# Kernel tuning notes

Hardware: AMD Instinct MI355X
Metric: run time of the kernel (lower is better)

Reference implementation:

```python
import jax, jax.numpy as jnp
import numpy as np

QTZ_BETA = 0.25


def setup_inputs() -> dict:
    key = jax.random.key(0)
    k1, k2 = jax.random.split(key)
    z = jax.random.normal(k1, (65536, 1, 256), dtype=jnp.float32)
    codebook = jax.random.normal(k2, (4096, 256), dtype=jnp.float32)
    return {"z": z, "codebook": codebook}


def reference(z, codebook):
    """Hard VQ quantization: nearest-codebook lookup with straight-through
    estimator plus codebook commitment loss. Returns (z_q, codebook_loss,
    min_embed_ids)."""
    D = codebook.shape[-1]
    z_f = z.reshape(-1, D)  # [N, D]
    # Pairwise squared L2 distances via expansion: ||z||^2 - 2 z c^T + ||c||^2
    # (argmin is invariant to the monotone transform vs. torch.cdist's sqrt)
    d2 = (
        jnp.sum(z_f * z_f, axis=1, keepdims=True)  # [N, 1]
        - 2.0 * (z_f @ codebook.T)                 # [N, K]
        + jnp.sum(codebook * codebook, axis=1)     # [K]
    )
    min_embed_ids = jnp.argmin(d2, axis=1)  # [N]
    # one_hot @ codebook is exactly a gather of codebook rows
    z_q = jnp.take(codebook, min_embed_ids, axis=0).reshape(z.shape)
    # Straight-through estimator
    z_q = z + jax.lax.stop_gradient(z_q - z)
    # Codebook loss (uses the STE z_q, matching the torch code)
    codebook_loss = (
        jnp.mean((jax.lax.stop_gradient(z_q) - z) ** 2)
        + jnp.mean((z_q - jax.lax.stop_gradient(z)) ** 2) * QTZ_BETA
    )
    return (z_q, codebook_loss, min_embed_ids)
```

## Files before the change

### kernel.cpp

```cpp
#include <hip/hip_runtime.h>
#include <stdint.h>

typedef _Float16 f16;
typedef _Float16 f16x4 __attribute__((ext_vector_type(4)));
typedef _Float16 f16x8 __attribute__((ext_vector_type(8)));
typedef float f32x4 __attribute__((ext_vector_type(4)));
typedef unsigned long long u64;

#define D_DIM 256
#define K_CB 4096
#define N_ROWS 65536
#define BM 128
#define BN 128
#define N_TILES 32
#define LOSS_OFF 16777216
#define IDS_OFF 16777217
#define MAX_FIX 4096

#define WS_CHI 0
#define WS_CN 2097152
#define WS_CNT 2113536
#define WS_ROWS 2113600
#define WS_SLOTS 2129984

#define LDS_BYTES 81920

#define GL_LDS(g, s_) __builtin_amdgcn_global_load_lds( \
    (const __attribute__((address_space(1))) void*)(g), \
    (__attribute__((address_space(3))) void*)(s_), 16, 0, 0)

static __device__ __forceinline__ uint32_t f2u(float x) { union { float f; uint32_t u; } c; c.f = x; return c.u; }
static __device__ __forceinline__ float u2f(uint32_t x) { union { float f; uint32_t u; } c; c.u = x; return c.f; }
static __device__ __forceinline__ uint32_t umin_(uint32_t a, uint32_t b) { return a < b ? a : b; }
static __device__ __forceinline__ uint32_t umax_(uint32_t a, uint32_t b) { return a > b ? a : b; }
static __device__ __forceinline__ u64 d2u(double x) { union { double d; u64 u; } c; c.d = x; return c.u; }

static __device__ __forceinline__ uint32_t med3u(uint32_t a, uint32_t b, uint32_t c) {
    uint32_t d;
    asm("v_med3_u32 %0, %1, %2, %3" : "=v"(d) : "v"(a), "v"(b), "v"(c));
    return d;
}
static __device__ __forceinline__ uint32_t min3u(uint32_t a, uint32_t b, uint32_t c) {
    uint32_t d;
    asm("v_min3_u32 %0, %1, %2, %3" : "=v"(d) : "v"(a), "v"(b), "v"(c));
    return d;
}

#define INS3(s_, kk_) do { \
    const uint32_t kkv_ = (kk_); \
    const uint32_t n1_ = umin_(k1[s_], kkv_); \
    const uint32_t n2_ = med3u(kkv_, k1[s_], k2[s_]); \
    const uint32_t n3_ = med3u(kkv_, k2[s_], k3[s_]); \
    k1[s_] = n1_; k2[s_] = n2_; k3[s_] = n3_; \
} while (0)

__global__ __launch_bounds__(256) void k_prep_cb(const float* __restrict__ cb,
                                                 f16* __restrict__ chi,
                                                 float* __restrict__ cn,
                                                 uint32_t* __restrict__ cnt,
                                                 u64* __restrict__ slots,
                                                 float* __restrict__ loss_slot) {
    const int tid = threadIdx.x;
    const int w = tid >> 6, l = tid & 63;
    const int row = blockIdx.x * 4 + w;
    const float4 v = ((const float4*)cb)[row * 64 + l];
    f16x4 h4;
    h4[0] = (f16)v.x; h4[1] = (f16)v.y; h4[2] = (f16)v.z; h4[3] = (f16)v.w;
    float ss = v.x * v.x + v.y * v.y + v.z * v.z + v.w * v.w;
#pragma unroll
    for (int m = 32; m >= 1; m >>= 1) ss += __shfl_xor(ss, m);
    ((f16x4*)chi)[row * 64 + l] = h4;
    if (l == 0) cn[row] = ss;
    if (tid < 4) slots[blockIdx.x * 4 + tid] = 0xFFFFFFFFFFFFFFFFull;
    if (blockIdx.x == 0 && tid == 0) { *cnt = 0; *loss_slot = 0.0f; }
}

__global__ __launch_bounds__(512, 4) void k_main(const float* __restrict__ z,
                                                 const float* __restrict__ cb,
                                                 const f16* __restrict__ chi,
                                                 const float* __restrict__ cn,
                                                 uint32_t* __restrict__ cnt,
                                                 uint32_t* __restrict__ rows,
                                                 float* __restrict__ out) {
    extern __shared__ char smem[];
    const int tid = threadIdx.x;
    const int w = tid >> 6, l = tid & 63;
    const int wm = w >> 1, wn = w & 1;
    const int l15 = l & 15, qh = l >> 4;
    const int blk = blockIdx.x;
    const float* ztile = z + (size_t)blk * (BM * D_DIM);

    const int e0 = tid >> 2;
    const int q0 = (tid & 3) ^ ((e0 >> 1) & 3);
    const int offE = e0 * 256 + q0 * 8;

    {
        const f16* gh = chi + offE;
        char* bb = smem + 65536 + w * 1024;
        GL_LDS(gh, bb);
    }

#pragma unroll 4
    for (int p = 0; p < 16; ++p) {
        const int r = p * 8 + w;
        const float4 v = ((const float4*)ztile)[r * 64 + l];
        f16x4 h4;
        h4[0] = (f16)(v.x * -2.0f); h4[1] = (f16)(v.y * -2.0f);
        h4[2] = (f16)(v.z * -2.0f); h4[3] = (f16)(v.w * -2.0f);
        const int kcw = l >> 3, q = (l >> 1) & 3, half = l & 1;
        const int addr = kcw * 8192 + r * 64 + (((q ^ ((r >> 1) & 3))) << 4) + half * 8;
        *(f16x4*)(smem + addr) = h4;
    }

    float cnNext[4];
#pragma unroll
    for (int j = 0; j < 4; ++j) cnNext[j] = cn[wn * 64 + j * 16 + l15];

    const int ab = wm * 2048 + l15 * 64 + ((qh ^ ((l15 >> 1) & 3)) << 4);

    int bcon[4];
#pragma unroll
    for (int j = 0; j < 4; ++j) {
        const int e = wn * 64 + j * 16 + l15;
        bcon[j] = e * 64 + ((qh ^ ((e >> 1) & 3)) << 4);
    }

    uint32_t k1[8], k2[8], k3[8];
#pragma unroll
    for (int s = 0; s < 8; ++s) { k1[s] = 0xFFFFFFFFu; k2[s] = 0xFFFFFFFFu; k3[s] = 0xFFFFFFFFu; }

    f32x4 acc[2][4];

    __syncthreads();

    for (int tile = 0; tile < N_TILES; ++tile) {
#pragma unroll
        for (int j = 0; j < 4; ++j) {
            const float base = cnNext[j] + 64.0f;
#pragma unroll
            for (int i = 0; i < 2; ++i) acc[i][j] = (f32x4){base, base, base, base};
        }
#pragma unroll
        for (int kc = 0; kc < 8; ++kc) {
            const int step = tile * 8 + kc;
            asm volatile("s_waitcnt vmcnt(0)" ::: "memory");
            __builtin_amdgcn_s_barrier();
            __builtin_amdgcn_sched_barrier(0);
            if (step + 1 < N_TILES * 8) {
                const int nt = (step + 1) >> 3, nk = (step + 1) & 7;
                const f16* gh = chi + nt * (BN * D_DIM) + nk * 32 + offE;
                char* bb = smem + 65536 + ((kc + 1) & 1) * 8192 + w * 1024;
                GL_LDS(gh, bb);
            }
            if (kc == 0) {
                const int tn = (tile + 1 < N_TILES) ? tile + 1 : tile;
#pragma unroll
                for (int j = 0; j < 4; ++j)
                    cnNext[j] = cn[tn * BN + wn * 64 + j * 16 + l15];
            }
            const char* bbase = smem + 65536 + (kc & 1) * 8192;
            f16x8 ah[2], bh[4];
#pragma unroll
            for (int i = 0; i < 2; ++i)
                ah[i] = *(const f16x8*)(smem + ab + kc * 8192 + i * 1024);
#pragma unroll
            for (int j = 0; j < 4; ++j) bh[j] = *(const f16x8*)(bbase + bcon[j]);
#pragma unroll
            for (int i = 0; i < 2; ++i)
#pragma unroll
                for (int j = 0; j < 4; ++j)
                    acc[i][j] = __builtin_amdgcn_mfma_f32_16x16x32_f16(ah[i], bh[j], acc[i][j], 0, 0, 0);
        }
        const int colb = tile * BN + wn * 64 + l15;
#pragma unroll
        for (int j = 0; j < 4; ++j) {
            const uint32_t col = (uint32_t)(colb + j * 16);
#pragma unroll
            for (int i = 0; i < 2; ++i)
#pragma unroll
                for (int rr = 0; rr < 4; ++rr) {
                    const uint32_t kk = (f2u(acc[i][j][rr]) & 0xFFFFF000u) | col;
                    INS3(i * 4 + rr, kk);
                }
        }
    }

#pragma unroll
    for (int s = 0; s < 8; ++s) {
        uint32_t a1 = k1[s], a2 = k2[s], a3 = k3[s];
#pragma unroll
        for (int m = 1; m <= 8; m <<= 1) {
            const uint32_t b1 = (uint32_t)__shfl_xor((int)a1, m);
            const uint32_t b2 = (uint32_t)__shfl_xor((int)a2, m);
            const uint32_t b3 = (uint32_t)__shfl_xor((int)a3, m);
            const uint32_t r1 = umin_(a1, b1);
            const uint32_t r2 = min3u(a2, b2, umax_(a1, b1));
            const uint32_t r3 = min3u(umax_(a1, b2), umax_(a2, b1), umin_(a3, b3));
            a1 = r1; a2 = r2; a3 = r3;
        }
        k1[s] = a1; k2[s] = a2; k3[s] = a3;
    }
    __syncthreads();
    uint32_t* mk = (uint32_t*)(smem + 65536);
    double* lossW = (double*)(smem + 65536 + 1536);
    if (wn == 0 && l15 == 0) {
#pragma unroll
        for (int s = 0; s < 8; ++s) {
            const int row = wm * 32 + (s >> 2) * 16 + qh * 4 + (s & 3);
            mk[row] = k1[s]; mk[128 + row] = k2[s]; mk[256 + row] = k3[s];
        }
    }
    __syncthreads();
    if (wn == 1 && l15 == 0) {
#pragma unroll
        for (int s = 0; s < 8; ++s) {
            const int row = wm * 32 + (s >> 2) * 16 + qh * 4 + (s & 3);
            const uint32_t b1 = mk[row], b2 = mk[128 + row], b3 = mk[256 + row];
            mk[row] = umin_(k1[s], b1);
            mk[128 + row] = min3u(k2[s], b2, umax_(k1[s], b1));
            mk[256 + row] = min3u(umax_(k1[s], b2), umax_(k2[s], b1), umin_(k3[s], b3));
        }
    }
    __syncthreads();

    double lossAcc = 0.0;
    for (int it = 0; it < 16; ++it) {
        const int row = it * 8 + w;
        const uint32_t K1 = mk[row], K2 = mk[128 + row], K3 = mk[256 + row];
        const int col1 = (int)(K1 & 4095u), col2 = (int)(K2 & 4095u);
        const float4 c1 = ((const float4*)cb)[col1 * 64 + l];
        const float4 c2 = ((const float4*)cb)[col2 * 64 + l];
        const float4 z4 = ((const float4*)ztile)[row * 64 + l];
        double e1, e2;
        {
            const double dx1 = (double)c1.x - z4.x, dy1 = (double)c1.y - z4.y;
            const double dz1 = (double)c1.z - z4.z, dw1 = (double)c1.w - z4.w;
            e1 = dx1 * dx1 + dy1 * dy1 + dz1 * dz1 + dw1 * dw1;
            const double dx2 = (double)c2.x - z4.x, dy2 = (double)c2.y - z4.y;
            const double dz2 = (double)c2.z - z4.z, dw2 = (double)c2.w - z4.w;
            e2 = dx2 * dx2 + dy2 * dy2 + dz2 * dz2 + dw2 * dw2;
        }
        float zn2 = z4.x * z4.x + z4.y * z4.y + z4.z * z4.z + z4.w * z4.w;
#pragma unroll
        for (int m = 32; m >= 1; m >>= 1) {
            e1 += __shfl_xor(e1, m);
            e2 += __shfl_xor(e2, m);
            zn2 += __shfl_xor(zn2, m);
        }
        const bool take1 = (e1 < e2) || (e1 == e2 && col1 <= col2);
        const float4 cw = take1 ? c1 : c2;
        ((float4*)out)[(blk * BM + row) * 64 + l] = cw;
        if (l == 0) {
            const int colw = take1 ? col1 : col2;
            const double ew = take1 ? e1 : e2;
            out[IDS_OFF + blk * BM + row] = (float)colw;
            lossAcc += ew;
            const float d3 = u2f(K3 & 0xFFFFF000u) + zn2 - 64.0f;
            const float eps = 0.006f * sqrtf(zn2) + 0.01f;
            if (!((float)ew < d3 - eps)) {
                const uint32_t e = atomicAdd(cnt, 1u);
                if (e < MAX_FIX) rows[e] = (uint32_t)(blk * BM + row);
            }
        }
    }
    if (l == 0) lossW[w] = lossAcc;
    __syncthreads();
    if (tid == 0) {
        double tot = 0.0;
#pragma unroll
        for (int i = 0; i < 8; ++i) tot += lossW[i];
        atomicAdd(out + LOSS_OFF, (float)(tot * (1.25 / 16777216.0)));
    }
}

__global__ __launch_bounds__(256) void k_fix_scan(const float* __restrict__ z,
                                                  const float* __restrict__ cb,
                                                  const uint32_t* __restrict__ cnt,
                                                  const uint32_t* __restrict__ rows,
                                                  u64* __restrict__ slots) {
    __shared__ float zrow[256];
    __shared__ u64 wmin[4];
    const int tid = threadIdx.x;
    const int w = tid >> 6, l = tid & 63;
    const int chunk = blockIdx.x & 15;
    uint32_t n = *cnt; if (n > MAX_FIX) n = MAX_FIX;
    for (uint32_t e = blockIdx.x >> 4; e < n; e += 64) {
        const int row = (int)rows[e];
        __syncthreads();
        if (tid < 64) ((float4*)zrow)[tid] = ((const float4*)z)[row * 64 + tid];
        __syncthreads();
        const int c = chunk * 256 + tid;
        const float4* crow = (const float4*)(cb + (size_t)c * 256);
        double s = 0.0;
        for (int q = 0; q < 64; ++q) {
            const float4 cv = crow[q];
            const float4 zv = ((const float4*)zrow)[q];
            const double dx = (double)cv.x - zv.x, dy = (double)cv.y - zv.y;
            const double dz = (double)cv.z - zv.z, dw = (double)cv.w - zv.w;
            s += dx * dx + dy * dy + dz * dz + dw * dw;
        }
        u64 key = (d2u(s) & 0xFFFFFFFFFFFFF000ull) | (u64)c;
#pragma unroll
        for (int m = 32; m >= 1; m >>= 1) {
            const u64 o = __shfl_xor(key, m);
            if (o < key) key = o;
        }
        if (l == 0) wmin[w] = key;
        __syncthreads();
        if (tid == 0) {
            u64 k = wmin[0];
            if (wmin[1] < k) k = wmin[1];
            if (wmin[2] < k) k = wmin[2];
            if (wmin[3] < k) k = wmin[3];
            atomicMin(&slots[e], k);
        }
    }
}

__global__ __launch_bounds__(256) void k_fix_patch(const float* __restrict__ z,
                                                   const float* __restrict__ cb,
                                                   const uint32_t* __restrict__ cnt,
                                                   const uint32_t* __restrict__ rows,
                                                   const u64* __restrict__ slots,
                                                   float* __restrict__ out) {
    const int tid = threadIdx.x;
    uint32_t n = *cnt; if (n > MAX_FIX) n = MAX_FIX;
    for (uint32_t e = blockIdx.x; e < n; e += 256) {
        const int row = (int)rows[e];
        const int newc = (int)(slots[e] & 4095ull);
        const int oldc = (int)out[IDS_OFF + row];
        if (newc == oldc) continue;
        double dOld = 0.0, dNew = 0.0;
        if (tid < 64) {
            const float4 zv = ((const float4*)z)[row * 64 + tid];
            const float4 co = ((const float4*)cb)[oldc * 64 + tid];
            const float4 cn4 = ((const float4*)cb)[newc * 64 + tid];
            const double ax = (double)co.x - zv.x, ay = (double)co.y - zv.y;
            const double az = (double)co.z - zv.z, aw = (double)co.w - zv.w;
            dOld = ax * ax + ay * ay + az * az + aw * aw;
            const double bx = (double)cn4.x - zv.x, by = (double)cn4.y - zv.y;
            const double bz = (double)cn4.z - zv.z, bw = (double)cn4.w - zv.w;
            dNew = bx * bx + by * by + bz * bz + bw * bw;
            ((float4*)out)[row * 64 + tid] = cn4;
        }
#pragma unroll
        for (int m = 32; m >= 1; m >>= 1) {
            dOld += __shfl_xor(dOld, m);
            dNew += __shfl_xor(dNew, m);
        }
        if (tid == 0) {
            out[IDS_OFF + row] = (float)newc;
            atomicAdd(out + LOSS_OFF, (float)((dNew - dOld) * (1.25 / 16777216.0)));
        }
    }
}

extern "C" void kernel_launch(void* const* d_in, const int* in_sizes, int n_in,
                              void* d_out, int out_size, void* d_ws, size_t ws_size,
                              hipStream_t stream) {
    (void)in_sizes; (void)n_in; (void)out_size; (void)ws_size;
    const float* z = (const float*)d_in[0];
    const float* cb = (const float*)d_in[1];
    float* out = (float*)d_out;
    char* ws = (char*)d_ws;
    f16* chi = (f16*)(ws + WS_CHI);
    float* cn = (float*)(ws + WS_CN);
    uint32_t* cnt = (uint32_t*)(ws + WS_CNT);
    uint32_t* rows = (uint32_t*)(ws + WS_ROWS);
    u64* slots = (u64*)(ws + WS_SLOTS);

    hipFuncSetAttribute((const void*)k_main,
                        hipFuncAttributeMaxDynamicSharedMemorySize, LDS_BYTES);

    k_prep_cb<<<K_CB / 4, 256, 0, stream>>>(cb, chi, cn, cnt, slots, out + LOSS_OFF);
    k_main<<<N_ROWS / BM, 512, LDS_BYTES, stream>>>(z, cb, chi, cn, cnt, rows, out);
    k_fix_scan<<<1024, 256, 0, stream>>>(z, cb, cnt, rows, slots);
    k_fix_patch<<<256, 256, 0, stream>>>(z, cb, cnt, rows, slots, out);
}
```

Baseline: 290.2 us.

## Use 16 waves per block with 4-stage codebook prefetch and LDS norms

Doubles the block to 1024 threads (16 waves in a 4x4 layout), so each wave computes a 32x32 sub-tile instead of 32x64. The codebook half-precision stream moves from double buffering to a 4-slot ring with prefetch three steps ahead and a relaxed vmcnt wait. All 4096 codebook norms are staged once in LDS rather than reloaded from global memory each tile. The top-3 candidate merge is extended across four column-waves with extra barriers. LDS use grows to 112 KB, which limits residency to one block per CU and halves the per-wave MFMA work between barriers.

```diff
diff --git a/kernel.cpp b/kernel.cpp
--- a/kernel.cpp
+++ b/kernel.cpp
@@ -23,7 +23,10 @@
 #define WS_ROWS 2113600
 #define WS_SLOTS 2129984
 
-#define LDS_BYTES 81920
+#define B_BASE 0
+#define CN_BASE 32768
+#define A_BASE 49152
+#define LDS_BYTES 114688
 
 #define GL_LDS(g, s_) __builtin_amdgcn_global_load_lds( \
     (const __attribute__((address_space(1))) void*)(g), \
@@ -75,17 +78,17 @@
     if (blockIdx.x == 0 && tid == 0) { *cnt = 0; *loss_slot = 0.0f; }
 }
 
-__global__ __launch_bounds__(512, 4) void k_main(const float* __restrict__ z,
-                                                 const float* __restrict__ cb,
-                                                 const f16* __restrict__ chi,
-                                                 const float* __restrict__ cn,
-                                                 uint32_t* __restrict__ cnt,
-                                                 uint32_t* __restrict__ rows,
-                                                 float* __restrict__ out) {
+__global__ __launch_bounds__(1024, 4) void k_main(const float* __restrict__ z,
+                                                  const float* __restrict__ cb,
+                                                  const f16* __restrict__ chi,
+                                                  const float* __restrict__ cn,
+                                                  uint32_t* __restrict__ cnt,
+                                                  uint32_t* __restrict__ rows,
+                                                  float* __restrict__ out) {
     extern __shared__ char smem[];
     const int tid = threadIdx.x;
     const int w = tid >> 6, l = tid & 63;
-    const int wm = w >> 1, wn = w & 1;
+    const int wm = w >> 2, wn = w & 3;
     const int l15 = l & 15, qh = l >> 4;
     const int blk = blockIdx.x;
     const float* ztile = z + (size_t)blk * (BM * D_DIM);
@@ -94,86 +97,81 @@
     const int q0 = (tid & 3) ^ ((e0 >> 1) & 3);
     const int offE = e0 * 256 + q0 * 8;
 
-    {
-        const f16* gh = chi + offE;
-        char* bb = smem + 65536 + w * 1024;
-        GL_LDS(gh, bb);
-    }
+    if (w < 8) {
+#pragma unroll
+        for (int s = 0; s < 3; ++s) {
+            const f16* gh = chi + s * 32 + offE;
+            GL_LDS(gh, smem + B_BASE + s * 8192 + w * 1024);
+        }
+    }
+
+    ((float4*)(smem + CN_BASE))[tid] = ((const float4*)cn)[tid];
 
 #pragma unroll 4
-    for (int p = 0; p < 16; ++p) {
-        const int r = p * 8 + w;
+    for (int p = 0; p < 8; ++p) {
+        const int r = p * 16 + w;
         const float4 v = ((const float4*)ztile)[r * 64 + l];
         f16x4 h4;
         h4[0] = (f16)(v.x * -2.0f); h4[1] = (f16)(v.y * -2.0f);
         h4[2] = (f16)(v.z * -2.0f); h4[3] = (f16)(v.w * -2.0f);
         const int kcw = l >> 3, q = (l >> 1) & 3, half = l & 1;
-        const int addr = kcw * 8192 + r * 64 + (((q ^ ((r >> 1) & 3))) << 4) + half * 8;
+        const int addr = A_BASE + kcw * 8192 + r * 64 + (((q ^ ((r >> 1) & 3))) << 4) + half * 8;
         *(f16x4*)(smem + addr) = h4;
     }
 
-    float cnNext[4];
-#pragma unroll
-    for (int j = 0; j < 4; ++j) cnNext[j] = cn[wn * 64 + j * 16 + l15];
-
-    const int ab = wm * 2048 + l15 * 64 + ((qh ^ ((l15 >> 1) & 3)) << 4);
-
-    int bcon[4];
-#pragma unroll
-    for (int j = 0; j < 4; ++j) {
-        const int e = wn * 64 + j * 16 + l15;
-        bcon[j] = e * 64 + ((qh ^ ((e >> 1) & 3)) << 4);
-    }
+    const int ab = A_BASE + wm * 2048 + l15 * 64 + ((qh ^ ((l15 >> 1) & 3)) << 4);
+
+    int bcon[2];
+#pragma unroll
+    for (int j = 0; j < 2; ++j) {
+        const int e = wn * 32 + j * 16 + l15;
+        bcon[j] = B_BASE + e * 64 + ((qh ^ ((l15 >> 1) & 3)) << 4);
+    }
+    int cnoff = CN_BASE + (wn * 32 + l15) * 4;
 
     uint32_t k1[8], k2[8], k3[8];
 #pragma unroll
     for (int s = 0; s < 8; ++s) { k1[s] = 0xFFFFFFFFu; k2[s] = 0xFFFFFFFFu; k3[s] = 0xFFFFFFFFu; }
 
-    f32x4 acc[2][4];
+    f32x4 acc[2][2];
 
     __syncthreads();
 
     for (int tile = 0; tile < N_TILES; ++tile) {
-#pragma unroll
-        for (int j = 0; j < 4; ++j) {
-            const float base = cnNext[j] + 64.0f;
-#pragma unroll
-            for (int i = 0; i < 2; ++i) acc[i][j] = (f32x4){base, base, base, base};
-        }
+        const float cb0 = *(const float*)(smem + cnoff) + 64.0f;
+        const float cb1 = *(const float*)(smem + cnoff + 64) + 64.0f;
+        cnoff += 512;
+        acc[0][0] = (f32x4){cb0, cb0, cb0, cb0};
+        acc[1][0] = acc[0][0];
+        acc[0][1] = (f32x4){cb1, cb1, cb1, cb1};
+        acc[1][1] = acc[0][1];
 #pragma unroll
         for (int kc = 0; kc < 8; ++kc) {
             const int step = tile * 8 + kc;
-            asm volatile("s_waitcnt vmcnt(0)" ::: "memory");
+            asm volatile("s_waitcnt vmcnt(2)" ::: "memory");
             __builtin_amdgcn_s_barrier();
             __builtin_amdgcn_sched_barrier(0);
-            if (step + 1 < N_TILES * 8) {
-                const int nt = (step + 1) >> 3, nk = (step + 1) & 7;
-                const f16* gh = chi + nt * (BN * D_DIM) + nk * 32 + offE;
-                char* bb = smem + 65536 + ((kc + 1) & 1) * 8192 + w * 1024;
-                GL_LDS(gh, bb);
+            if (w < 8) {
+                int s3 = step + 3; if (s3 > N_TILES * 8 - 1) s3 = N_TILES * 8 - 1;
+                const f16* gh = chi + (s3 >> 3) * (BN * D_DIM) + (s3 & 7) * 32 + offE;
+                GL_LDS(gh, smem + B_BASE + ((kc + 3) & 3) * 8192 + w * 1024);
             }
-            if (kc == 0) {
-                const int tn = (tile + 1 < N_TILES) ? tile + 1 : tile;
-#pragma unroll
-                for (int j = 0; j < 4; ++j)
-                    cnNext[j] = cn[tn * BN + wn * 64 + j * 16 + l15];
-            }
-            const char* bbase = smem + 65536 + (kc & 1) * 8192;
-            f16x8 ah[2], bh[4];
+            f16x8 ah[2], bh[2];
 #pragma unroll
             for (int i = 0; i < 2; ++i)
                 ah[i] = *(const f16x8*)(smem + ab + kc * 8192 + i * 1024);
 #pragma unroll
-            for (int j = 0; j < 4; ++j) bh[j] = *(const f16x8*)(bbase + bcon[j]);
+            for (int j = 0; j < 2; ++j)
+                bh[j] = *(const f16x8*)(smem + bcon[j] + (kc & 3) * 8192);
 #pragma unroll
             for (int i = 0; i < 2; ++i)
 #pragma unroll
-                for (int j = 0; j < 4; ++j)
+                for (int j = 0; j < 2; ++j)
                     acc[i][j] = __builtin_amdgcn_mfma_f32_16x16x32_f16(ah[i], bh[j], acc[i][j], 0, 0, 0);
         }
-        const int colb = tile * BN + wn * 64 + l15;
-#pragma unroll
-        for (int j = 0; j < 4; ++j) {
+        const int colb = tile * BN + wn * 32 + l15;
+#pragma unroll
+        for (int j = 0; j < 2; ++j) {
             const uint32_t col = (uint32_t)(colb + j * 16);
 #pragma unroll
             for (int i = 0; i < 2; ++i)
@@ -184,6 +182,7 @@
                 }
         }
     }
+    asm volatile("s_waitcnt vmcnt(0)" ::: "memory");
 
 #pragma unroll
     for (int s = 0; s < 8; ++s) {
@@ -201,8 +200,8 @@
         k1[s] = a1; k2[s] = a2; k3[s] = a3;
     }
     __syncthreads();
-    uint32_t* mk = (uint32_t*)(smem + 65536);
-    double* lossW = (double*)(smem + 65536 + 1536);
+    uint32_t* mk = (uint32_t*)(smem + CN_BASE);
+    double* lossW = (double*)(smem + CN_BASE + 1536);
     if (wn == 0 && l15 == 0) {
 #pragma unroll
         for (int s = 0; s < 8; ++s) {
@@ -210,22 +209,25 @@
             mk[row] = k1[s]; mk[128 + row] = k2[s]; mk[256 + row] = k3[s];
         }
     }
+#pragma unroll
+    for (int mw = 1; mw < 4; ++mw) {
+        __syncthreads();
+        if (wn == mw && l15 == 0) {
+#pragma unroll
+            for (int s = 0; s < 8; ++s) {
+                const int row = wm * 32 + (s >> 2) * 16 + qh * 4 + (s & 3);
+                const uint32_t b1 = mk[row], b2 = mk[128 + row], b3 = mk[256 + row];
+                mk[row] = umin_(k1[s], b1);
+                mk[128 + row] = min3u(k2[s], b2, umax_(k1[s], b1));
+                mk[256 + row] = min3u(umax_(k1[s], b2), umax_(k2[s], b1), umin_(k3[s], b3));
+            }
+        }
+    }
     __syncthreads();
-    if (wn == 1 && l15 == 0) {
-#pragma unroll
-        for (int s = 0; s < 8; ++s) {
-            const int row = wm * 32 + (s >> 2) * 16 + qh * 4 + (s & 3);
-            const uint32_t b1 = mk[row], b2 = mk[128 + row], b3 = mk[256 + row];
-            mk[row] = umin_(k1[s], b1);
-            mk[128 + row] = min3u(k2[s], b2, umax_(k1[s], b1));
-            mk[256 + row] = min3u(umax_(k1[s], b2), umax_(k2[s], b1), umin_(k3[s], b3));
-        }
-    }
-    __syncthreads();
 
     double lossAcc = 0.0;
-    for (int it = 0; it < 16; ++it) {
-        const int row = it * 8 + w;
+    for (int it = 0; it < 8; ++it) {
+        const int row = it * 16 + w;
         const uint32_t K1 = mk[row], K2 = mk[128 + row], K3 = mk[256 + row];
         const int col1 = (int)(K1 & 4095u), col2 = (int)(K2 & 4095u);
         const float4 c1 = ((const float4*)cb)[col1 * 64 + l];
@@ -268,7 +270,7 @@
     if (tid == 0) {
         double tot = 0.0;
 #pragma unroll
-        for (int i = 0; i < 8; ++i) tot += lossW[i];
+        for (int i = 0; i < 16; ++i) tot += lossW[i];
         atomicAdd(out + LOSS_OFF, (float)(tot * (1.25 / 16777216.0)));
     }
 }
@@ -373,7 +375,7 @@
                         hipFuncAttributeMaxDynamicSharedMemorySize, LDS_BYTES);
 
     k_prep_cb<<<K_CB / 4, 256, 0, stream>>>(cb, chi, cn, cnt, slots, out + LOSS_OFF);
-    k_main<<<N_ROWS / BM, 512, LDS_BYTES, stream>>>(z, cb, chi, cn, cnt, rows, out);
+    k_main<<<N_ROWS / BM, 1024, LDS_BYTES, stream>>>(z, cb, chi, cn, cnt, rows, out);
     k_fix_scan<<<1024, 256, 0, stream>>>(z, cb, cnt, rows, slots);
     k_fix_patch<<<256, 256, 0, stream>>>(z, cb, cnt, rows, slots, out);
 }
```

Result: slower. 307.3 us (+5.9%).

## Widen codebook tile to 256, deepen B prefetch pipeline, register double-buffer fragments

Applied to the files above, without the earlier changes.

Raises the per-block codebook tile from 128 to 256 columns and rearranges warps into a 2x4 grid, so each warp computes a 64x64 sub-tile with 16 accumulators and A fragments are reused across more MFMAs. B staging moves from 2 to 4 LDS buffers with loads issued three steps ahead and a partial vmcnt wait, so global-to-LDS copies overlap compute instead of draining every step. LDS fragments are double-buffered in registers, and codebook norms are staged in LDS once per block instead of re-read from global. The costs are much higher LDS use (144 KB) and register pressure, which cut occupancy to 2 blocks per CU, plus a longer serial top-3 merge across four column warps.

```diff
diff --git a/kernel.cpp b/kernel.cpp
--- a/kernel.cpp
+++ b/kernel.cpp
@@ -11,8 +11,9 @@
 #define K_CB 4096
 #define N_ROWS 65536
 #define BM 128
-#define BN 128
-#define N_TILES 32
+#define BN 256
+#define N_TILES 16
+#define N_STEPS 128
 #define LOSS_OFF 16777216
 #define IDS_OFF 16777217
 #define MAX_FIX 4096
@@ -23,7 +24,10 @@
 #define WS_ROWS 2113600
 #define WS_SLOTS 2129984
 
-#define LDS_BYTES 81920
+#define A_BASE 0
+#define B_BASE 65536
+#define CN_BASE 131072
+#define LDS_BYTES 147456
 
 #define GL_LDS(g, s_) __builtin_amdgcn_global_load_lds( \
     (const __attribute__((address_space(1))) void*)(g), \
@@ -75,7 +79,7 @@
     if (blockIdx.x == 0 && tid == 0) { *cnt = 0; *loss_slot = 0.0f; }
 }
 
-__global__ __launch_bounds__(512, 4) void k_main(const float* __restrict__ z,
+__global__ __launch_bounds__(512, 2) void k_main(const float* __restrict__ z,
                                                  const float* __restrict__ cb,
                                                  const f16* __restrict__ chi,
                                                  const float* __restrict__ cn,
@@ -85,20 +89,27 @@
     extern __shared__ char smem[];
     const int tid = threadIdx.x;
     const int w = tid >> 6, l = tid & 63;
-    const int wm = w >> 1, wn = w & 1;
+    const int wm = w >> 2, wn = w & 3;
     const int l15 = l & 15, qh = l >> 4;
     const int blk = blockIdx.x;
     const float* ztile = z + (size_t)blk * (BM * D_DIM);
 
-    const int e0 = tid >> 2;
-    const int q0 = (tid & 3) ^ ((e0 >> 1) & 3);
-    const int offE = e0 * 256 + q0 * 8;
-
-    {
-        const f16* gh = chi + offE;
-        char* bb = smem + 65536 + w * 1024;
-        GL_LDS(gh, bb);
-    }
+    const int e_lo = (w << 4) + (l >> 2);
+    const int swq = ((l & 3) ^ ((l >> 3) & 3)) << 3;
+    const int offE0 = e_lo * 256 + swq;
+    const int offE1 = offE0 + 32768;
+    const int stg0 = w * 1024;
+    const int stg1 = stg0 + 8192;
+
+#pragma unroll
+    for (int s = 0; s < 3; ++s) {
+        const f16* gh = chi + s * 32;
+        GL_LDS(gh + offE0, smem + B_BASE + s * 16384 + stg0);
+        GL_LDS(gh + offE1, smem + B_BASE + s * 16384 + stg1);
+    }
+
+    ((float4*)(smem + CN_BASE))[tid] = ((const float4*)cn)[tid];
+    ((float4*)(smem + CN_BASE))[tid + 512] = ((const float4*)cn)[tid + 512];
 
 #pragma unroll 4
     for (int p = 0; p < 16; ++p) {
@@ -108,75 +119,67 @@
         h4[0] = (f16)(v.x * -2.0f); h4[1] = (f16)(v.y * -2.0f);
         h4[2] = (f16)(v.z * -2.0f); h4[3] = (f16)(v.w * -2.0f);
         const int kcw = l >> 3, q = (l >> 1) & 3, half = l & 1;
-        const int addr = kcw * 8192 + r * 64 + (((q ^ ((r >> 1) & 3))) << 4) + half * 8;
+        const int addr = A_BASE + kcw * 8192 + r * 64 + (((q ^ ((r >> 1) & 3))) << 4) + half * 8;
         *(f16x4*)(smem + addr) = h4;
     }
 
-    float cnNext[4];
-#pragma unroll
-    for (int j = 0; j < 4; ++j) cnNext[j] = cn[wn * 64 + j * 16 + l15];
-
-    const int ab = wm * 2048 + l15 * 64 + ((qh ^ ((l15 >> 1) & 3)) << 4);
-
-    int bcon[4];
-#pragma unroll
-    for (int j = 0; j < 4; ++j) {
-        const int e = wn * 64 + j * 16 + l15;
-        bcon[j] = e * 64 + ((qh ^ ((e >> 1) & 3)) << 4);
-    }
-
-    uint32_t k1[8], k2[8], k3[8];
-#pragma unroll
-    for (int s = 0; s < 8; ++s) { k1[s] = 0xFFFFFFFFu; k2[s] = 0xFFFFFFFFu; k3[s] = 0xFFFFFFFFu; }
-
-    f32x4 acc[2][4];
+    const int ab = A_BASE + wm * 4096 + l15 * 64 + ((qh ^ ((l15 >> 1) & 3)) << 4);
+    const int bb0 = B_BASE + wn * 4096 + l15 * 64 + ((qh ^ ((l15 >> 1) & 3)) << 4);
+
+    uint32_t k1[16], k2[16], k3[16];
+#pragma unroll
+    for (int s = 0; s < 16; ++s) { k1[s] = 0xFFFFFFFFu; k2[s] = 0xFFFFFFFFu; k3[s] = 0xFFFFFFFFu; }
+
+    f32x4 acc[4][4];
+    f16x8 pA[4], pB[4], qA[4], qB[4];
 
     __syncthreads();
 
+#pragma unroll
+    for (int i = 0; i < 4; ++i) pA[i] = *(const f16x8*)(smem + ab + i * 1024);
+#pragma unroll
+    for (int j = 0; j < 4; ++j) pB[j] = *(const f16x8*)(smem + bb0 + j * 1024);
+
+#define K_STEP(kc_, CA, CB, NA, NB) do { \
+    asm volatile("s_waitcnt vmcnt(2)" ::: "memory"); \
+    __builtin_amdgcn_s_barrier(); \
+    __builtin_amdgcn_sched_barrier(0); \
+    { int s3 = tile * 8 + (kc_) + 3; if (s3 > N_STEPS - 1) s3 = N_STEPS - 1; \
+      const f16* gh_ = chi + (s3 >> 3) * (BN * D_DIM) + (s3 & 7) * 32; \
+      char* bb_ = smem + B_BASE + (((kc_) + 3) & 3) * 16384; \
+      GL_LDS(gh_ + offE0, bb_ + stg0); \
+      GL_LDS(gh_ + offE1, bb_ + stg1); } \
+    _Pragma("unroll") for (int i = 0; i < 4; ++i) \
+        NA[i] = *(const f16x8*)(smem + ab + (((kc_) + 1) & 7) * 8192 + i * 1024); \
+    _Pragma("unroll") for (int j = 0; j < 4; ++j) \
+        NB[j] = *(const f16x8*)(smem + bb0 + (((kc_) + 1) & 3) * 16384 + j * 1024); \
+    _Pragma("unroll") for (int i = 0; i < 4; ++i) \
+        _Pragma("unroll") for (int j = 0; j < 4; ++j) \
+            acc[i][j] = __builtin_amdgcn_mfma_f32_16x16x32_f16(CA[i], CB[j], acc[i][j], 0, 0, 0); \
+} while (0)
+
     for (int tile = 0; tile < N_TILES; ++tile) {
+        const int cnb = CN_BASE + tile * 1024 + wn * 256 + l15 * 4;
 #pragma unroll
         for (int j = 0; j < 4; ++j) {
-            const float base = cnNext[j] + 64.0f;
-#pragma unroll
-            for (int i = 0; i < 2; ++i) acc[i][j] = (f32x4){base, base, base, base};
-        }
-#pragma unroll
-        for (int kc = 0; kc < 8; ++kc) {
-            const int step = tile * 8 + kc;
-            asm volatile("s_waitcnt vmcnt(0)" ::: "memory");
-            __builtin_amdgcn_s_barrier();
-            __builtin_amdgcn_sched_barrier(0);
-            if (step + 1 < N_TILES * 8) {
-                const int nt = (step + 1) >> 3, nk = (step + 1) & 7;
-                const f16* gh = chi + nt * (BN * D_DIM) + nk * 32 + offE;
-                char* bb = smem + 65536 + ((kc + 1) & 1) * 8192 + w * 1024;
-                GL_LDS(gh, bb);
-            }
-            if (kc == 0) {
-                const int tn = (tile + 1 < N_TILES) ? tile + 1 : tile;
-#pragma unroll
-                for (int j = 0; j < 4; ++j)
-                    cnNext[j] = cn[tn * BN + wn * 64 + j * 16 + l15];
-            }
-            const char* bbase = smem + 65536 + (kc & 1) * 8192;
-            f16x8 ah[2], bh[4];
-#pragma unroll
-            for (int i = 0; i < 2; ++i)
-                ah[i] = *(const f16x8*)(smem + ab + kc * 8192 + i * 1024);
-#pragma unroll
-            for (int j = 0; j < 4; ++j) bh[j] = *(const f16x8*)(bbase + bcon[j]);
-#pragma unroll
-            for (int i = 0; i < 2; ++i)
-#pragma unroll
-                for (int j = 0; j < 4; ++j)
-                    acc[i][j] = __builtin_amdgcn_mfma_f32_16x16x32_f16(ah[i], bh[j], acc[i][j], 0, 0, 0);
-        }
+            const float base = *(const float*)(smem + cnb + j * 64) + 64.0f;
+#pragma unroll
+            for (int i = 0; i < 4; ++i) acc[i][j] = (f32x4){base, base, base, base};
+        }
+        K_STEP(0, pA, pB, qA, qB);
+        K_STEP(1, qA, qB, pA, pB);
+        K_STEP(2, pA, pB, qA, qB);
+        K_STEP(3, qA, qB, pA, pB);
+        K_STEP(4, pA, pB, qA, qB);
+        K_STEP(5, qA, qB, pA, pB);
+        K_STEP(6, pA, pB, qA, qB);
+        K_STEP(7, qA, qB, pA, pB);
         const int colb = tile * BN + wn * 64 + l15;
 #pragma unroll
         for (int j = 0; j < 4; ++j) {
             const uint32_t col = (uint32_t)(colb + j * 16);
 #pragma unroll
-            for (int i = 0; i < 2; ++i)
+            for (int i = 0; i < 4; ++i)
 #pragma unroll
                 for (int rr = 0; rr < 4; ++rr) {
                     const uint32_t kk = (f2u(acc[i][j][rr]) & 0xFFFFF000u) | col;
@@ -184,9 +187,11 @@
                 }
         }
     }
-
-#pragma unroll
-    for (int s = 0; s < 8; ++s) {
+#undef K_STEP
+    asm volatile("s_waitcnt vmcnt(0)" ::: "memory");
+
+#pragma unroll
+    for (int s = 0; s < 16; ++s) {
         uint32_t a1 = k1[s], a2 = k2[s], a3 = k3[s];
 #pragma unroll
         for (int m = 1; m <= 8; m <<= 1) {
@@ -201,24 +206,27 @@
         k1[s] = a1; k2[s] = a2; k3[s] = a3;
     }
     __syncthreads();
-    uint32_t* mk = (uint32_t*)(smem + 65536);
-    double* lossW = (double*)(smem + 65536 + 1536);
+    uint32_t* mk = (uint32_t*)(smem + CN_BASE);
+    double* lossW = (double*)(smem + CN_BASE + 1536);
     if (wn == 0 && l15 == 0) {
 #pragma unroll
-        for (int s = 0; s < 8; ++s) {
-            const int row = wm * 32 + (s >> 2) * 16 + qh * 4 + (s & 3);
+        for (int s = 0; s < 16; ++s) {
+            const int row = wm * 64 + (s >> 2) * 16 + qh * 4 + (s & 3);
             mk[row] = k1[s]; mk[128 + row] = k2[s]; mk[256 + row] = k3[s];
         }
     }
-    __syncthreads();
-    if (wn == 1 && l15 == 0) {
-#pragma unroll
-        for (int s = 0; s < 8; ++s) {
-            const int row = wm * 32 + (s >> 2) * 16 + qh * 4 + (s & 3);
-            const uint32_t b1 = mk[row], b2 = mk[128 + row], b3 = mk[256 + row];
-            mk[row] = umin_(k1[s], b1);
-            mk[128 + row] = min3u(k2[s], b2, umax_(k1[s], b1));
-            mk[256 + row] = min3u(umax_(k1[s], b2), umax_(k2[s], b1), umin_(k3[s], b3));
+#pragma unroll
+    for (int mw = 1; mw < 4; ++mw) {
+        __syncthreads();
+        if (wn == mw && l15 == 0) {
+#pragma unroll
+            for (int s = 0; s < 16; ++s) {
+                const int row = wm * 64 + (s >> 2) * 16 + qh * 4 + (s & 3);
+                const uint32_t b1 = mk[row], b2 = mk[128 + row], b3 = mk[256 + row];
+                mk[row] = umin_(k1[s], b1);
+                mk[128 + row] = min3u(k2[s], b2, umax_(k1[s], b1));
+                mk[256 + row] = min3u(umax_(k1[s], b2), umax_(k2[s], b1), umin_(k3[s], b3));
+            }
         }
     }
     __syncthreads();
```

Result: no change. 296.0 us (+2.0%).

## Stream codebook fragments directly into registers with 4-stage prefetch, drop per-step barriers

Applied to the files above, without the earlier changes.

The main GEMM-argmin kernel drops from 8 to 4 waves per block, and each wave now covers 64 rows instead of 32. Codebook B fragments are no longer staged through LDS with global_load_lds and a barrier every k-step. Instead each wave loads them straight from global memory into a 4-deep register ring, prefetching three steps ahead. The A fragments are double-buffered in registers, and all codebook norms are preloaded into LDS. This removes the per-step vmcnt waits and workgroup barriers, but each wave now loads its own B data from global or L2 rather than sharing it, and register pressure rises.

```diff
diff --git a/kernel.cpp b/kernel.cpp
--- a/kernel.cpp
+++ b/kernel.cpp
@@ -13,6 +13,7 @@
 #define BM 128
 #define BN 128
 #define N_TILES 32
+#define N_STEPS 256
 #define LOSS_OFF 16777216
 #define IDS_OFF 16777217
 #define MAX_FIX 4096
@@ -23,11 +24,9 @@
 #define WS_ROWS 2113600
 #define WS_SLOTS 2129984
 
+#define A_BASE 0
+#define CN_BASE 65536
 #define LDS_BYTES 81920
-
-#define GL_LDS(g, s_) __builtin_amdgcn_global_load_lds( \
-    (const __attribute__((address_space(1))) void*)(g), \
-    (__attribute__((address_space(3))) void*)(s_), 16, 0, 0)
 
 static __device__ __forceinline__ uint32_t f2u(float x) { union { float f; uint32_t u; } c; c.f = x; return c.u; }
 static __device__ __forceinline__ float u2f(uint32_t x) { union { float f; uint32_t u; } c; c.u = x; return c.f; }
@@ -75,7 +74,7 @@
     if (blockIdx.x == 0 && tid == 0) { *cnt = 0; *loss_slot = 0.0f; }
 }
 
-__global__ __launch_bounds__(512, 4) void k_main(const float* __restrict__ z,
+__global__ __launch_bounds__(256, 2) void k_main(const float* __restrict__ z,
                                                  const float* __restrict__ cb,
                                                  const f16* __restrict__ chi,
                                                  const float* __restrict__ cn,
@@ -90,93 +89,92 @@
     const int blk = blockIdx.x;
     const float* ztile = z + (size_t)blk * (BM * D_DIM);
 
-    const int e0 = tid >> 2;
-    const int q0 = (tid & 3) ^ ((e0 >> 1) & 3);
-    const int offE = e0 * 256 + q0 * 8;
-
-    {
-        const f16* gh = chi + offE;
-        char* bb = smem + 65536 + w * 1024;
-        GL_LDS(gh, bb);
-    }
+    int vOffB[4];
+#pragma unroll
+    for (int j = 0; j < 4; ++j)
+        vOffB[j] = (wn * 64 + j * 16 + l15) * 512 + qh * 16;
+
+    f16x8 bhR[4][4];
+#pragma unroll
+    for (int s = 0; s < 3; ++s) {
+        const char* gb = (const char*)chi + s * 64;
+#pragma unroll
+        for (int j = 0; j < 4; ++j)
+            bhR[s][j] = *(const f16x8*)(gb + vOffB[j]);
+    }
+
+#pragma unroll
+    for (int c4 = 0; c4 < 4; ++c4)
+        ((float4*)(smem + CN_BASE))[c4 * 256 + tid] = ((const float4*)cn)[c4 * 256 + tid];
 
 #pragma unroll 4
-    for (int p = 0; p < 16; ++p) {
-        const int r = p * 8 + w;
+    for (int p = 0; p < 32; ++p) {
+        const int r = p * 4 + w;
         const float4 v = ((const float4*)ztile)[r * 64 + l];
         f16x4 h4;
         h4[0] = (f16)(v.x * -2.0f); h4[1] = (f16)(v.y * -2.0f);
         h4[2] = (f16)(v.z * -2.0f); h4[3] = (f16)(v.w * -2.0f);
         const int kcw = l >> 3, q = (l >> 1) & 3, half = l & 1;
-        const int addr = kcw * 8192 + r * 64 + (((q ^ ((r >> 1) & 3))) << 4) + half * 8;
+        const int addr = A_BASE + kcw * 8192 + r * 64 + (((q ^ ((r >> 1) & 3))) << 4) + half * 8;
         *(f16x4*)(smem + addr) = h4;
     }
 
+    const int ab = A_BASE + wm * 4096 + l15 * 64 + ((qh ^ ((l15 >> 1) & 3)) << 4);
+    const int cnA = CN_BASE + (wn * 64 + l15) * 4;
+
+    uint32_t k1[16], k2[16], k3[16];
+#pragma unroll
+    for (int s = 0; s < 16; ++s) { k1[s] = 0xFFFFFFFFu; k2[s] = 0xFFFFFFFFu; k3[s] = 0xFFFFFFFFu; }
+
+    f32x4 acc[4][4];
+    f16x8 ah[2][4];
     float cnNext[4];
-#pragma unroll
-    for (int j = 0; j < 4; ++j) cnNext[j] = cn[wn * 64 + j * 16 + l15];
-
-    const int ab = wm * 2048 + l15 * 64 + ((qh ^ ((l15 >> 1) & 3)) << 4);
-
-    int bcon[4];
-#pragma unroll
-    for (int j = 0; j < 4; ++j) {
-        const int e = wn * 64 + j * 16 + l15;
-        bcon[j] = e * 64 + ((qh ^ ((e >> 1) & 3)) << 4);
-    }
-
-    uint32_t k1[8], k2[8], k3[8];
-#pragma unroll
-    for (int s = 0; s < 8; ++s) { k1[s] = 0xFFFFFFFFu; k2[s] = 0xFFFFFFFFu; k3[s] = 0xFFFFFFFFu; }
-
-    f32x4 acc[2][4];
-
-    __syncthreads();
+
+    __syncthreads();
+
+#pragma unroll
+    for (int j = 0; j < 4; ++j) cnNext[j] = *(const float*)(smem + cnA + j * 64);
+#pragma unroll
+    for (int i = 0; i < 4; ++i) ah[0][i] = *(const f16x8*)(smem + ab + i * 1024);
 
     for (int tile = 0; tile < N_TILES; ++tile) {
 #pragma unroll
         for (int j = 0; j < 4; ++j) {
             const float base = cnNext[j] + 64.0f;
 #pragma unroll
-            for (int i = 0; i < 2; ++i) acc[i][j] = (f32x4){base, base, base, base};
+            for (int i = 0; i < 4; ++i) acc[i][j] = (f32x4){base, base, base, base};
         }
 #pragma unroll
         for (int kc = 0; kc < 8; ++kc) {
-            const int step = tile * 8 + kc;
-            asm volatile("s_waitcnt vmcnt(0)" ::: "memory");
-            __builtin_amdgcn_s_barrier();
-            __builtin_amdgcn_sched_barrier(0);
-            if (step + 1 < N_TILES * 8) {
-                const int nt = (step + 1) >> 3, nk = (step + 1) & 7;
-                const f16* gh = chi + nt * (BN * D_DIM) + nk * 32 + offE;
-                char* bb = smem + 65536 + ((kc + 1) & 1) * 8192 + w * 1024;
-                GL_LDS(gh, bb);
+            {
+                int s3 = tile * 8 + kc + 3;
+                if (s3 > N_STEPS - 1) s3 = N_STEPS - 1;
+                const char* gb = (const char*)chi + ((s3 >> 3) << 16) + ((s3 & 7) << 6);
+#pragma unroll
+                for (int j = 0; j < 4; ++j)
+                    bhR[(kc + 3) & 3][j] = *(const f16x8*)(gb + vOffB[j]);
             }
+#pragma unroll
+            for (int i = 0; i < 4; ++i)
+                ah[(kc + 1) & 1][i] = *(const f16x8*)(smem + ab + (((kc + 1) & 7) * 8192) + i * 1024);
             if (kc == 0) {
                 const int tn = (tile + 1 < N_TILES) ? tile + 1 : tile;
 #pragma unroll
                 for (int j = 0; j < 4; ++j)
-                    cnNext[j] = cn[tn * BN + wn * 64 + j * 16 + l15];
+                    cnNext[j] = *(const float*)(smem + cnA + tn * 512 + j * 64);
             }
-            const char* bbase = smem + 65536 + (kc & 1) * 8192;
-            f16x8 ah[2], bh[4];
-#pragma unroll
-            for (int i = 0; i < 2; ++i)
-                ah[i] = *(const f16x8*)(smem + ab + kc * 8192 + i * 1024);
-#pragma unroll
-            for (int j = 0; j < 4; ++j) bh[j] = *(const f16x8*)(bbase + bcon[j]);
-#pragma unroll
-            for (int i = 0; i < 2; ++i)
+#pragma unroll
+            for (int i = 0; i < 4; ++i)
 #pragma unroll
                 for (int j = 0; j < 4; ++j)
-                    acc[i][j] = __builtin_amdgcn_mfma_f32_16x16x32_f16(ah[i], bh[j], acc[i][j], 0, 0, 0);
+                    acc[i][j] = __builtin_amdgcn_mfma_f32_16x16x32_f16(ah[kc & 1][i], bhR[kc & 3][j], acc[i][j], 0, 0, 0);
         }
         const int colb = tile * BN + wn * 64 + l15;
 #pragma unroll
         for (int j = 0; j < 4; ++j) {
             const uint32_t col = (uint32_t)(colb + j * 16);
 #pragma unroll
-            for (int i = 0; i < 2; ++i)
+            for (int i = 0; i < 4; ++i)
 #pragma unroll
                 for (int rr = 0; rr < 4; ++rr) {
                     const uint32_t kk = (f2u(acc[i][j][rr]) & 0xFFFFF000u) | col;
@@ -186,7 +184,7 @@
     }
 
 #pragma unroll
-    for (int s = 0; s < 8; ++s) {
+    for (int s = 0; s < 16; ++s) {
         uint32_t a1 = k1[s], a2 = k2[s], a3 = k3[s];
 #pragma unroll
         for (int m = 1; m <= 8; m <<= 1) {
@@ -201,20 +199,20 @@
         k1[s] = a1; k2[s] = a2; k3[s] = a3;
     }
     __syncthreads();
-    uint32_t* mk = (uint32_t*)(smem + 65536);
-    double* lossW = (double*)(smem + 65536 + 1536);
+    uint32_t* mk = (uint32_t*)(smem + CN_BASE);
+    double* lossW = (double*)(smem + CN_BASE + 1536);
     if (wn == 0 && l15 == 0) {
 #pragma unroll
-        for (int s = 0; s < 8; ++s) {
-            const int row = wm * 32 + (s >> 2) * 16 + qh * 4 + (s & 3);
+        for (int s = 0; s < 16; ++s) {
+            const int row = wm * 64 + (s >> 2) * 16 + qh * 4 + (s & 3);
             mk[row] = k1[s]; mk[128 + row] = k2[s]; mk[256 + row] = k3[s];
         }
     }
     __syncthreads();
     if (wn == 1 && l15 == 0) {
 #pragma unroll
-        for (int s = 0; s < 8; ++s) {
-            const int row = wm * 32 + (s >> 2) * 16 + qh * 4 + (s & 3);
+        for (int s = 0; s < 16; ++s) {
+            const int row = wm * 64 + (s >> 2) * 16 + qh * 4 + (s & 3);
             const uint32_t b1 = mk[row], b2 = mk[128 + row], b3 = mk[256 + row];
             mk[row] = umin_(k1[s], b1);
             mk[128 + row] = min3u(k2[s], b2, umax_(k1[s], b1));
@@ -224,8 +222,8 @@
     __syncthreads();
 
     double lossAcc = 0.0;
-    for (int it = 0; it < 16; ++it) {
-        const int row = it * 8 + w;
+    for (int it = 0; it < 32; ++it) {
+        const int row = it * 4 + w;
         const uint32_t K1 = mk[row], K2 = mk[128 + row], K3 = mk[256 + row];
         const int col1 = (int)(K1 & 4095u), col2 = (int)(K2 & 4095u);
         const float4 c1 = ((const float4*)cb)[col1 * 64 + l];
@@ -266,10 +264,8 @@
     if (l == 0) lossW[w] = lossAcc;
     __syncthreads();
     if (tid == 0) {
-        double tot = 0.0;
-#pragma unroll
-        for (int i = 0; i < 8; ++i) tot += lossW[i];
-        atomicAdd(out + LOSS_OFF, (float)(tot * (1.25 / 16777216.0)));
+        const double tot = (lossW[0] + lossW[1] + lossW[2] + lossW[3]) * (1.25 / 16777216.0);
+        atomicAdd(out + LOSS_OFF, (float)tot);
     }
 }
 
@@ -373,7 +369,7 @@
                         hipFuncAttributeMaxDynamicSharedMemorySize, LDS_BYTES);
 
     k_prep_cb<<<K_CB / 4, 256, 0, stream>>>(cb, chi, cn, cnt, slots, out + LOSS_OFF);
-    k_main<<<N_ROWS / BM, 512, LDS_BYTES, stream>>>(z, cb, chi, cn, cnt, rows, out);
+    k_main<<<N_ROWS / BM, 256, LDS_BYTES, stream>>>(z, cb, chi, cn, cnt, rows, out);
     k_fix_scan<<<1024, 256, 0, stream>>>(z, cb, cnt, rows, slots);
     k_fix_patch<<<256, 256, 0, stream>>>(z, cb, cnt, rows, slots, out);
 }
```

Result: slower. 508.4 us (+75.2%).
